# Kernel optimization log

Measured on AMD Instinct MI355X. Metric: run time of the kernel, lower is better.

Reference implementation:

```python
import jax, jax.numpy as jnp
import numpy as np

N, E = 100000, 1600000
IN_C, HID, OUT = 128, 64, 25
EPS = 1e-5


def gcn_conv(x, row, col, W, b):
    # PyG GCNConv: h = x@W; add self-loops; sym-norm D^-1/2 A D^-1/2; + bias
    h = x @ W                                   # [N, F]
    ones = jnp.ones(row.shape[0], h.dtype)
    deg = jax.ops.segment_sum(ones, col, num_segments=N) + 1.0  # +1 self-loop
    dinv = jax.lax.rsqrt(deg)                   # [N]
    norm = dinv[row] * dinv[col]                # [E]
    agg = jax.ops.segment_sum(h[row] * norm[:, None], col, num_segments=N)
    agg = agg + (dinv * dinv)[:, None] * h      # self-loop contribution
    return agg + b


def layer_norm(x, w, b):
    # PyG LayerNorm mode='node': normalize each node over feature dim
    mu = jnp.mean(x, axis=-1, keepdims=True)
    var = jnp.var(x, axis=-1, keepdims=True)
    return (x - mu) * jax.lax.rsqrt(var + EPS) * w + b


def setup_inputs() -> dict:
    key = jax.random.key(0)
    ks = jax.random.split(key, 16)
    x = jax.random.normal(ks[0], (N, IN_C), dtype=jnp.float32)
    edge_index = jax.random.randint(ks[1], (2, E), 0, N, dtype=jnp.int32)

    def glorot(k, shp):
        lim = float(np.sqrt(6.0 / (shp[0] + shp[1])))
        return jax.random.uniform(k, shp, jnp.float32, -lim, lim)

    return {
        "x": x,
        "edge_index": edge_index,
        "W1": glorot(ks[2], (IN_C, HID)), "b1": jnp.zeros((HID,), jnp.float32),
        "W2": glorot(ks[3], (HID, HID)), "b2": jnp.zeros((HID,), jnp.float32),
        "W3": glorot(ks[4], (HID, HID)), "b3": jnp.zeros((HID,), jnp.float32),
        "ln1_w": jnp.ones((HID,), jnp.float32), "ln1_b": jnp.zeros((HID,), jnp.float32),
        "ln2_w": jnp.ones((HID,), jnp.float32), "ln2_b": jnp.zeros((HID,), jnp.float32),
        "ln3_w": jnp.ones((HID,), jnp.float32), "ln3_b": jnp.zeros((HID,), jnp.float32),
        "Wl": glorot(ks[5], (HID, OUT)), "bl": jnp.zeros((OUT,), jnp.float32),
    }


def reference(x, edge_index, W1, b1, W2, b2, W3, b3,
              ln1_w, ln1_b, ln2_w, ln2_b, ln3_w, ln3_b, Wl, bl):
    row, col = edge_index[0], edge_index[1]
    h = jax.nn.relu(layer_norm(gcn_conv(x, row, col, W1, b1), ln1_w, ln1_b))
    h = jax.nn.relu(layer_norm(gcn_conv(h, row, col, W2, b2), ln2_w, ln2_b))
    h = jax.nn.relu(layer_norm(gcn_conv(h, row, col, W3, b3), ln3_w, ln3_b))
    pooled = jnp.mean(h, axis=0)                # [HID]
    return pooled @ Wl + bl                     # [OUT]
```

## Files before the change

kernel.cpp:

```cpp
#include <hip/hip_runtime.h>
#include <hip/hip_bf16.h>

typedef __hip_bfloat16 bf16;
typedef __attribute__((ext_vector_type(8))) short short8;
typedef __attribute__((ext_vector_type(4))) float f32x4;
typedef __attribute__((ext_vector_type(2))) float f32x2;

#define HID 64
#define CAP 4096
#define BSH 7
#define EPB 2048

__device__ __forceinline__ unsigned short f2bfbits(float x){
    union { float f; unsigned u; } c; c.f = x;
    unsigned r = c.u + 0x7fffu + ((c.u >> 16) & 1u);
    return (unsigned short)(r >> 16);
}
__device__ __forceinline__ unsigned char f2fp8(float x){
    unsigned v = __builtin_amdgcn_cvt_pk_fp8_f32(x, x, 0u, false);
    return (unsigned char)(v & 0xffu);
}
template<bool HI>
__device__ __forceinline__ f32x2 cvtpk(unsigned u){
    return __builtin_amdgcn_cvt_pk_f32_fp8(u, HI);
}


__global__ __launch_bounds__(1024) void bin_kernel(const int* __restrict__ row,
                                                   const int* __restrict__ col,
                                                   int E, int NB,
                                                   int* __restrict__ gCur,
                                                   int* __restrict__ binned,
                                                   unsigned char* __restrict__ H8a,
                                                   unsigned char* __restrict__ H8b,
                                                   int N){
    __shared__ int lCnt[1024];
    __shared__ int lOff[1024];
    __shared__ int lGB[1024];
    __shared__ int sPay[EPB];
    __shared__ unsigned short sB[EPB];
    __shared__ int wSum[16];
    int tid = threadIdx.x;
    int lane = tid & 63, wv = tid >> 6;
    if (blockIdx.x == 0 && tid < 32){
        unsigned* za = (unsigned*)(H8a + ((size_t)N << 6));
        unsigned* zb = (unsigned*)(H8b + ((size_t)N << 6));
        if (tid < 16) za[tid] = 0u; else zb[tid - 16] = 0u;
    }
    int e0 = blockIdx.x * EPB;
    int eN = E - e0; if (eN > EPB) eN = EPB;

    lCnt[tid] = 0;
    int cols[2], rows[2];
    #pragma unroll
    for (int k = 0; k < 2; ++k){
        int i = tid + k * 1024;
        bool ok = (i < eN);
        cols[k] = ok ? col[e0 + i] : -1;
        rows[k] = ok ? row[e0 + i] : 0;
    }
    __syncthreads();
    #pragma unroll
    for (int k = 0; k < 2; ++k)
        if (cols[k] >= 0) atomicAdd(&lCnt[cols[k] >> BSH], 1);
    __syncthreads();

    int c = lCnt[tid];
    int inc = c;
    #pragma unroll
    for (int m = 1; m < 64; m <<= 1){
        int t = __shfl_up(inc, m);
        if (lane >= m) inc += t;
    }
    if (lane == 63) wSum[wv] = inc;
    __syncthreads();
    if (wv == 0 && lane < 16){
        int orig = wSum[lane];
        int ws = orig;
        #pragma unroll
        for (int m = 1; m < 16; m <<= 1){
            int t = __shfl_up(ws, m);
            if (lane >= m) ws += t;
        }
        wSum[lane] = ws - orig;
    }
    __syncthreads();
    int excl = inc - c + wSum[wv];
    lOff[tid] = excl;
    if (c){
        int gb = atomicAdd(&gCur[tid], c);
        lGB[tid] = tid * CAP + gb - excl;
    }
    lCnt[tid] = 0;
    __syncthreads();

    #pragma unroll
    for (int k = 0; k < 2; ++k){
        if (cols[k] >= 0){
            int bk = cols[k] >> BSH;
            int rk = atomicAdd(&lCnt[bk], 1);
            int pos = lOff[bk] + rk;
            sPay[pos] = ((cols[k] & 127) << 17) | rows[k];
            sB[pos] = (unsigned short)bk;
        }
    }
    __syncthreads();

    #pragma unroll
    for (int k = 0; k < 2; ++k){
        int i = tid + k * 1024;
        if (i < eN){
            int bk = sB[i];
            int tgt = lGB[bk] + i;
            if (tgt - (bk << 12) < CAP)
                binned[tgt] = sPay[i];
        }
    }
}


template<int K, typename T>
__global__ __launch_bounds__(256) void matmul_kernel(const T* __restrict__ act,
                                                     const float* __restrict__ W,
                                                     const int* __restrict__ gCur,
                                                     const int* __restrict__ binned,
                                                     int* __restrict__ col_ptr,
                                                     int* __restrict__ cnt,
                                                     unsigned char* __restrict__ H8, int N){
    constexpr int KS = K / 32;
    constexpr int RB = 2 * K;
    __shared__ __align__(16) short As[128 * K];
    __shared__ __align__(16) short Wt[64 * K];
    __shared__ int fineCnt[128];
    __shared__ int scW[2];

    int tid = threadIdx.x;
    int b = blockIdx.x;
    int nodeBase = b * 128;
    int j0g = b * CAP;
    int cB = gCur[b];
    if (cB > CAP) cB = CAP;

    if (tid < 128) fineCnt[tid] = 0;

    for (int i = tid; i < K * 64; i += 256){
        int k = i >> 6, c = i & 63;
        unsigned short bb = f2bfbits(W[i]);
        int byte = c * RB + ((2 * k) ^ ((c & 7) << 4));
        *(short*)((char*)Wt + byte) = (short)bb;
    }
    constexpr int OPR = K / 8;
    for (int i = tid; i < 128 * OPR; i += 256){
        int node = i / OPR, oct = i % OPR;
        int n = nodeBase + node;
        short8 v = (short8)0;
        if (n < N){
            if constexpr (sizeof(T) == 4){
                const float4* xp = (const float4*)&act[(size_t)n * K + oct * 8];
                float4 a = xp[0], bb = xp[1];
                v[0] = (short)f2bfbits(a.x); v[1] = (short)f2bfbits(a.y);
                v[2] = (short)f2bfbits(a.z); v[3] = (short)f2bfbits(a.w);
                v[4] = (short)f2bfbits(bb.x); v[5] = (short)f2bfbits(bb.y);
                v[6] = (short)f2bfbits(bb.z); v[7] = (short)f2bfbits(bb.w);
            } else {
                v = *(const short8*)&act[(size_t)n * K + oct * 8];
            }
        }
        int byte = node * RB + ((oct * 16) ^ ((node & 7) << 4));
        *(short8*)((char*)As + byte) = v;
    }
    __syncthreads();

    for (int i = tid; i < cB; i += 256)
        atomicAdd(&fineCnt[binned[j0g + i] >> 17], 1);
    __syncthreads();
    int cf = 0, inc = 0;
    if (tid < 128){
        cf = fineCnt[tid];
        inc = cf;
        #pragma unroll
        for (int m = 1; m < 64; m <<= 1){
            int t = __shfl_up(inc, m);
            if ((tid & 63) >= m) inc += t;
        }
        if ((tid & 63) == 63) scW[tid >> 6] = inc;
    }
    __syncthreads();
    if (tid < 128){
        int off = (tid >= 64) ? scW[0] : 0;
        int node = nodeBase + tid;
        if (node < N){
            col_ptr[node] = j0g + off + inc - cf;
            cnt[node] = cf;
        }
    }
    __syncthreads();

    int wv = tid >> 6, l = tid & 63;
    int lr = l & 15, lg = l >> 4;

    short8 bfr[KS][4];
    #pragma unroll
    for (int ks = 0; ks < KS; ++ks)
        #pragma unroll
        for (int t = 0; t < 4; ++t){
            int c = t * 16 + lr;
            int byte = c * RB + ((ks * 64 + lg * 16) ^ ((c & 7) << 4));
            bfr[ks][t] = *(const short8*)((const char*)Wt + byte);
        }

    #pragma unroll
    for (int nt = 0; nt < 2; ++nt){
        int nb = wv * 32 + nt * 16;
        int node = nb + lr;
        short8 af[KS];
        #pragma unroll
        for (int ks = 0; ks < KS; ++ks){
            int byte = node * RB + ((ks * 64 + lg * 16) ^ ((node & 7) << 4));
            af[ks] = *(const short8*)((const char*)As + byte);
        }
        f32x4 acc[4] = {(f32x4)0.f, (f32x4)0.f, (f32x4)0.f, (f32x4)0.f};
        #pragma unroll
        for (int ks = 0; ks < KS; ++ks)
            #pragma unroll
            for (int t = 0; t < 4; ++t)
                acc[t] = __builtin_amdgcn_mfma_f32_16x16x32_bf16(af[ks], bfr[ks][t], acc[t], 0, 0, 0);
        #pragma unroll
        for (int r = 0; r < 4; ++r){
            int loc = nb + lg * 4 + r;
            int n = nodeBase + loc;
            if (n < N){
                float dv = rsqrtf((float)fineCnt[loc] + 1.0f);
                #pragma unroll
                for (int t = 0; t < 4; ++t)
                    H8[((size_t)(unsigned)n << 6) + t * 16 + lr] = f2fp8(acc[t][r] * dv);
            }
        }
    }
}


__global__ __launch_bounds__(512) void agg_sort_kernel(const unsigned char* __restrict__ H8in,
                                                       const int* __restrict__ cnt,
                                                       const int* __restrict__ gCur,
                                                       const int* __restrict__ binned,
                                                       const int* __restrict__ col_ptr,
                                                       int* __restrict__ csr_row,
                                                       const float* __restrict__ bias,
                                                       const float* __restrict__ lnw,
                                                       const float* __restrict__ lnb,
                                                       const float* __restrict__ Wn,
                                                       unsigned char* __restrict__ H8out,
                                                       int N){
    __shared__ int sCsr[CAP];
    __shared__ __align__(16) short ybuf[8192];
    __shared__ __align__(16) short Wt[4096];
    __shared__ int fineCur[128];
    __shared__ float sdv[128];
    int b = blockIdx.x, tid = threadIdx.x;
    int wid = tid >> 6, l = tid & 63;
    int g = l >> 2, s = l & 3;
    int nodeBase = b << BSH;
    int n = nodeBase + wid * 16 + g;
    bool valid = (n < N);
    int nc = valid ? n : N;

    int j0g = b * CAP;
    int cntB = gCur[b];
    if (cntB > CAP) cntB = CAP;

    for (int i = tid; i < 4096; i += 512){
        int k = i >> 6, c = i & 63;
        unsigned short bb = f2bfbits(Wn[i]);
        int byte = c * 128 + ((2 * k) ^ ((c & 7) << 4));
        *(short*)((char*)Wt + byte) = (short)bb;
    }
    if (tid < 128){
        int node = nodeBase + tid;
        fineCur[tid] = (node < N) ? (col_ptr[node] - j0g) : 0;
    }
    __syncthreads();

    for (int i = tid; i < cntB; i += 512){
        int w = binned[j0g + i];
        int pos = atomicAdd(&fineCur[w >> 17], 1);
        sCsr[pos] = w & 0x1FFFF;
    }
    __syncthreads();
    for (int i = tid; i < cntB; i += 512) csr_row[j0g + i] = sCsr[i];

    int deg = valid ? cnt[nc] : 0;
    int p = valid ? (col_ptr[nc] - j0g) : 0;
    unsigned soff = (unsigned)(s << 4);
    const char* Hb = (const char*)H8in;
    uint4 us = *(const uint4*)(Hb + ((((unsigned)nc) << 6) | soff));

    int mdeg = deg;
    mdeg = max(mdeg, __shfl_xor(mdeg, 4));
    mdeg = max(mdeg, __shfl_xor(mdeg, 8));
    mdeg = max(mdeg, __shfl_xor(mdeg, 16));
    mdeg = max(mdeg, __shfl_xor(mdeg, 32));

    f32x2 a0 = {0.f,0.f}, a1 = {0.f,0.f}, a2 = {0.f,0.f}, a3 = {0.f,0.f};
    f32x2 a4 = {0.f,0.f}, a5 = {0.f,0.f}, a6 = {0.f,0.f}, a7 = {0.f,0.f};
#define ACC4(u) { a0 += cvtpk<false>((u).x); a1 += cvtpk<true>((u).x); \
                  a2 += cvtpk<false>((u).y); a3 += cvtpk<true>((u).y); \
                  a4 += cvtpk<false>((u).z); a5 += cvtpk<true>((u).z); \
                  a6 += cvtpk<false>((u).w); a7 += cvtpk<true>((u).w); }
    for (int i = 0; i < mdeg; i += 4){
        int r0 = (i     < deg) ? sCsr[p + i    ] : N;
        int r1 = (i + 1 < deg) ? sCsr[p + i + 1] : N;
        int r2 = (i + 2 < deg) ? sCsr[p + i + 2] : N;
        int r3 = (i + 3 < deg) ? sCsr[p + i + 3] : N;
        uint4 u0 = *(const uint4*)(Hb + ((((unsigned)r0) << 6) | soff));
        uint4 u1 = *(const uint4*)(Hb + ((((unsigned)r1) << 6) | soff));
        uint4 u2 = *(const uint4*)(Hb + ((((unsigned)r2) << 6) | soff));
        uint4 u3 = *(const uint4*)(Hb + ((((unsigned)r3) << 6) | soff));
        ACC4(u0) ACC4(u1) ACC4(u2) ACC4(u3)
    }
#undef ACC4
    a0 += cvtpk<false>(us.x); a1 += cvtpk<true>(us.x);
    a2 += cvtpk<false>(us.y); a3 += cvtpk<true>(us.y);
    a4 += cvtpk<false>(us.z); a5 += cvtpk<true>(us.z);
    a6 += cvtpk<false>(us.w); a7 += cvtpk<true>(us.w);

    float dv = rsqrtf((float)deg + 1.0f);
    float acc16[16] = { a0.x, a0.y, a1.x, a1.y, a2.x, a2.y, a3.x, a3.y,
                        a4.x, a4.y, a5.x, a5.y, a6.x, a6.y, a7.x, a7.y };
    float v[16], y[16];
    float4 bq[4], wq[4], cq[4];
    #pragma unroll
    for (int q = 0; q < 4; ++q){
        bq[q] = ((const float4*)bias)[(s << 2) + q];
        wq[q] = ((const float4*)lnw)[(s << 2) + q];
        cq[q] = ((const float4*)lnb)[(s << 2) + q];
    }
    #pragma unroll
    for (int j = 0; j < 16; ++j)
        v[j] = fmaf(dv, acc16[j], ((const float*)&bq[j >> 2])[j & 3]);
    float sum = 0.f;
    #pragma unroll
    for (int j = 0; j < 16; ++j) sum += v[j];
    sum += __shfl_xor(sum, 1); sum += __shfl_xor(sum, 2);
    float mu = sum * (1.0f / 64.0f);
    float var = 0.f;
    #pragma unroll
    for (int j = 0; j < 16; ++j){ float d = v[j] - mu; var = fmaf(d, d, var); }
    var += __shfl_xor(var, 1); var += __shfl_xor(var, 2);
    float rstd = rsqrtf(var * (1.0f / 64.0f) + 1e-5f);
    #pragma unroll
    for (int j = 0; j < 16; ++j){
        float d = (v[j] - mu) * rstd;
        y[j] = fmaxf(fmaf(d, ((const float*)&wq[j >> 2])[j & 3],
                             ((const float*)&cq[j >> 2])[j & 3]), 0.0f);
    }

    if (s == 0) sdv[(wid << 4) + g] = dv;
    char* yb = (char*)ybuf;
    int base = (wid << 11) + (g << 7);
    int sw = (g & 7) << 4;
    short8 ya, yz;
    #pragma unroll
    for (int j = 0; j < 8; ++j){ ya[j] = (short)f2bfbits(y[j]); yz[j] = (short)f2bfbits(y[8 + j]); }
    *(short8*)(yb + base + (((s << 5)     ) ^ sw)) = ya;
    *(short8*)(yb + base + (((s << 5) + 16) ^ sw)) = yz;

    int lr = l & 15, lg = l >> 4;
    short8 bfr[2][4];
    #pragma unroll
    for (int ks = 0; ks < 2; ++ks)
        #pragma unroll
        for (int t = 0; t < 4; ++t){
            int c = t * 16 + lr;
            int byte = c * 128 + ((((ks << 2) + lg) << 4) ^ ((c & 7) << 4));
            bfr[ks][t] = *(const short8*)((const char*)Wt + byte);
        }
    short8 af[2];
    #pragma unroll
    for (int ks = 0; ks < 2; ++ks){
        int byte = (wid << 11) + lr * 128 + ((((ks << 2) + lg) << 4) ^ ((lr & 7) << 4));
        af[ks] = *(const short8*)(yb + byte);
    }
    f32x4 acc[4] = {(f32x4)0.f, (f32x4)0.f, (f32x4)0.f, (f32x4)0.f};
    #pragma unroll
    for (int ks = 0; ks < 2; ++ks)
        #pragma unroll
        for (int t = 0; t < 4; ++t)
            acc[t] = __builtin_amdgcn_mfma_f32_16x16x32_bf16(af[ks], bfr[ks][t], acc[t], 0, 0, 0);
    #pragma unroll
    for (int r = 0; r < 4; ++r){
        int nn = nodeBase + (wid << 4) + (lg << 2) + r;
        if (nn < N){
            float dv2 = sdv[(wid << 4) + (lg << 2) + r];
            #pragma unroll
            for (int t = 0; t < 4; ++t)
                H8out[((size_t)(unsigned)nn << 6) + t * 16 + lr] = f2fp8(acc[t][r] * dv2);
        }
    }
}


template<bool POOL>
__global__ __launch_bounds__(256) void agg_kernel(const unsigned char* __restrict__ H8in,
                                                  const int* __restrict__ cnt,
                                                  const int* __restrict__ col_ptr,
                                                  const int* __restrict__ csr_row,
                                                  const float* __restrict__ bias,
                                                  const float* __restrict__ lnw,
                                                  const float* __restrict__ lnb,
                                                  const float* __restrict__ Wn,
                                                  unsigned char* __restrict__ H8out,
                                                  float* __restrict__ pooledRep, int N){
    __shared__ int sIdx[CAP];
    __shared__ __align__(16) short ybuf[POOL ? 8 : 4096];
    __shared__ __align__(16) short Wt[POOL ? 8 : 4096];
    __shared__ float sp[POOL ? 256 : 4];
    __shared__ float sdv[64];
    int tid = threadIdx.x;
    int wid = tid >> 6, l = tid & 63;
    int g = l >> 2, s = l & 3;
    int nodeBase = blockIdx.x * 64;
    int n = nodeBase + wid * 16 + g;
    bool valid = (n < N);
    int nc = valid ? n : N;

    int lastN = nodeBase + 63; if (lastN > N - 1) lastN = N - 1;
    int jlo = col_ptr[nodeBase];
    int jhi = col_ptr[lastN] + cnt[lastN];
    int cntR = jhi - jlo;

    int deg = valid ? cnt[n] : 0;
    int p = valid ? (col_ptr[n] - jlo) : 0;

    for (int i = tid; i < cntR; i += 256) sIdx[i] = csr_row[jlo + i];
    if (!POOL){
        for (int i = tid; i < 4096; i += 256){
            int k = i >> 6, c = i & 63;
            unsigned short bb = f2bfbits(Wn[i]);
            int byte = c * 128 + ((2 * k) ^ ((c & 7) << 4));
            *(short*)((char*)Wt + byte) = (short)bb;
        }
    }
    __syncthreads();

    unsigned soff = (unsigned)(s << 4);
    const char* Hb = (const char*)H8in;
    uint4 us = *(const uint4*)(Hb + ((((unsigned)nc) << 6) | soff));

    int mdeg = deg;
    mdeg = max(mdeg, __shfl_xor(mdeg, 4));
    mdeg = max(mdeg, __shfl_xor(mdeg, 8));
    mdeg = max(mdeg, __shfl_xor(mdeg, 16));
    mdeg = max(mdeg, __shfl_xor(mdeg, 32));

    f32x2 a0 = {0.f,0.f}, a1 = {0.f,0.f}, a2 = {0.f,0.f}, a3 = {0.f,0.f};
    f32x2 a4 = {0.f,0.f}, a5 = {0.f,0.f}, a6 = {0.f,0.f}, a7 = {0.f,0.f};
#define ACC4(u) { a0 += cvtpk<false>((u).x); a1 += cvtpk<true>((u).x); \
                  a2 += cvtpk<false>((u).y); a3 += cvtpk<true>((u).y); \
                  a4 += cvtpk<false>((u).z); a5 += cvtpk<true>((u).z); \
                  a6 += cvtpk<false>((u).w); a7 += cvtpk<true>((u).w); }
    for (int i = 0; i < mdeg; i += 4){
        int r0 = (i     < deg) ? sIdx[p + i    ] : N;
        int r1 = (i + 1 < deg) ? sIdx[p + i + 1] : N;
        int r2 = (i + 2 < deg) ? sIdx[p + i + 2] : N;
        int r3 = (i + 3 < deg) ? sIdx[p + i + 3] : N;
        uint4 u0 = *(const uint4*)(Hb + ((((unsigned)r0) << 6) | soff));
        uint4 u1 = *(const uint4*)(Hb + ((((unsigned)r1) << 6) | soff));
        uint4 u2 = *(const uint4*)(Hb + ((((unsigned)r2) << 6) | soff));
        uint4 u3 = *(const uint4*)(Hb + ((((unsigned)r3) << 6) | soff));
        ACC4(u0) ACC4(u1) ACC4(u2) ACC4(u3)
    }
#undef ACC4
    a0 += cvtpk<false>(us.x); a1 += cvtpk<true>(us.x);
    a2 += cvtpk<false>(us.y); a3 += cvtpk<true>(us.y);
    a4 += cvtpk<false>(us.z); a5 += cvtpk<true>(us.z);
    a6 += cvtpk<false>(us.w); a7 += cvtpk<true>(us.w);

    float dv = rsqrtf((float)deg + 1.0f);
    float acc16[16] = { a0.x, a0.y, a1.x, a1.y, a2.x, a2.y, a3.x, a3.y,
                        a4.x, a4.y, a5.x, a5.y, a6.x, a6.y, a7.x, a7.y };
    float v[16], y[16];
    float4 bq[4], wq[4], cq[4];
    #pragma unroll
    for (int q = 0; q < 4; ++q){
        bq[q] = ((const float4*)bias)[(s << 2) + q];
        wq[q] = ((const float4*)lnw)[(s << 2) + q];
        cq[q] = ((const float4*)lnb)[(s << 2) + q];
    }
    #pragma unroll
    for (int j = 0; j < 16; ++j)
        v[j] = fmaf(dv, acc16[j], ((const float*)&bq[j >> 2])[j & 3]);
    float sum = 0.f;
    #pragma unroll
    for (int j = 0; j < 16; ++j) sum += v[j];
    sum += __shfl_xor(sum, 1); sum += __shfl_xor(sum, 2);
    float mu = sum * (1.0f / 64.0f);
    float var = 0.f;
    #pragma unroll
    for (int j = 0; j < 16; ++j){ float d = v[j] - mu; var = fmaf(d, d, var); }
    var += __shfl_xor(var, 1); var += __shfl_xor(var, 2);
    float rstd = rsqrtf(var * (1.0f / 64.0f) + 1e-5f);
    #pragma unroll
    for (int j = 0; j < 16; ++j){
        float d = (v[j] - mu) * rstd;
        y[j] = fmaxf(fmaf(d, ((const float*)&wq[j >> 2])[j & 3],
                             ((const float*)&cq[j >> 2])[j & 3]), 0.0f);
    }

    if (POOL){
        #pragma unroll
        for (int j = 0; j < 16; ++j){
            float z = valid ? y[j] : 0.f;
            z += __shfl_xor(z, 4); z += __shfl_xor(z, 8);
            z += __shfl_xor(z, 16); z += __shfl_xor(z, 32);
            y[j] = z;
        }
        if (l < 4){
            #pragma unroll
            for (int q = 0; q < 4; ++q)
                ((float4*)sp)[wid * 16 + (s << 2) + q] =
                    make_float4(y[4*q], y[4*q+1], y[4*q+2], y[4*q+3]);
        }
        __syncthreads();
        if (tid < 64){
            float t = sp[tid] + sp[64 + tid] + sp[128 + tid] + sp[192 + tid];
            atomicAdd(&pooledRep[(blockIdx.x & 63) * 64 + tid], t);
        }
    } else {
        if (s == 0) sdv[(wid << 4) + g] = dv;
        char* yb = (char*)ybuf;
        int base = (wid << 11) + (g << 7);
        int sw = (g & 7) << 4;
        short8 ya, yz;
        #pragma unroll
        for (int j = 0; j < 8; ++j){ ya[j] = (short)f2bfbits(y[j]); yz[j] = (short)f2bfbits(y[8 + j]); }
        *(short8*)(yb + base + (((s << 5)     ) ^ sw)) = ya;
        *(short8*)(yb + base + (((s << 5) + 16) ^ sw)) = yz;

        int lr = l & 15, lg = l >> 4;
        short8 bfr[2][4];
        #pragma unroll
        for (int ks = 0; ks < 2; ++ks)
            #pragma unroll
            for (int t = 0; t < 4; ++t){
                int c = t * 16 + lr;
                int byte = c * 128 + ((((ks << 2) + lg) << 4) ^ ((c & 7) << 4));
                bfr[ks][t] = *(const short8*)((const char*)Wt + byte);
            }
        short8 af[2];
        #pragma unroll
        for (int ks = 0; ks < 2; ++ks){
            int byte = (wid << 11) + lr * 128 + ((((ks << 2) + lg) << 4) ^ ((lr & 7) << 4));
            af[ks] = *(const short8*)(yb + byte);
        }
        f32x4 acc[4] = {(f32x4)0.f, (f32x4)0.f, (f32x4)0.f, (f32x4)0.f};
        #pragma unroll
        for (int ks = 0; ks < 2; ++ks)
            #pragma unroll
            for (int t = 0; t < 4; ++t)
                acc[t] = __builtin_amdgcn_mfma_f32_16x16x32_bf16(af[ks], bfr[ks][t], acc[t], 0, 0, 0);
        #pragma unroll
        for (int r = 0; r < 4; ++r){
            int nn = nodeBase + (wid << 4) + (lg << 2) + r;
            if (nn < N){
                float dv2 = sdv[(wid << 4) + (lg << 2) + r];
                #pragma unroll
                for (int t = 0; t < 4; ++t)
                    H8out[((size_t)(unsigned)nn << 6) + t * 16 + lr] = f2fp8(acc[t][r] * dv2);
            }
        }
    }
}


__global__ __launch_bounds__(64) void final_kernel(const float* __restrict__ pooledRep,
                                                   const float* __restrict__ Wl,
                                                   const float* __restrict__ bl,
                                                   float* __restrict__ outp, float invN){
    __shared__ float pooled[64];
    int t = threadIdx.x;
    float s = 0.f;
    #pragma unroll 8
    for (int r = 0; r < 64; ++r) s += pooledRep[r * 64 + t];
    pooled[t] = s;
    __syncthreads();
    if (t < 25){
        float acc = bl[t];
        #pragma unroll 8
        for (int f = 0; f < HID; ++f)
            acc = fmaf(pooled[f] * invN, Wl[f * 25 + t], acc);
        outp[t] = acc;
    }
}


static inline size_t alignup(size_t x){ return (x + 255) & ~(size_t)255; }

extern "C" void kernel_launch(void* const* d_in, const int* in_sizes, int n_in,
                              void* d_out, int out_size, void* d_ws, size_t ws_size,
                              hipStream_t stream) {
    const float* x   = (const float*)d_in[0];
    const int*   ei  = (const int*)d_in[1];
    const float* W1  = (const float*)d_in[2];
    const float* b1  = (const float*)d_in[3];
    const float* W2  = (const float*)d_in[4];
    const float* b2  = (const float*)d_in[5];
    const float* W3  = (const float*)d_in[6];
    const float* b3  = (const float*)d_in[7];
    const float* ln1w = (const float*)d_in[8];
    const float* ln1b = (const float*)d_in[9];
    const float* ln2w = (const float*)d_in[10];
    const float* ln2b = (const float*)d_in[11];
    const float* ln3w = (const float*)d_in[12];
    const float* ln3b = (const float*)d_in[13];
    const float* Wl  = (const float*)d_in[14];
    const float* bl  = (const float*)d_in[15];

    const int N = in_sizes[0] / 128;
    const int E = in_sizes[1] / 2;
    const int NB = (N + 127) >> BSH;
    const int* row = ei;
    const int* col = ei + E;

    char* p = (char*)d_ws;
    int*   gCur      = (int*)p;   p += alignup((size_t)NB * 4);
    float* pooledRep = (float*)p; p += alignup(64 * 64 * 4);
    size_t zeroBytes = (size_t)((char*)p - (char*)gCur);
    int*   binned    = (int*)p;   p += alignup((size_t)NB * CAP * 4);
    int*   csr_row   = (int*)p;   p += alignup((size_t)NB * CAP * 4);
    int*   col_ptr   = (int*)p;   p += alignup((size_t)N * 4);
    int*   cnt       = (int*)p;   p += alignup((size_t)N * 4);
    unsigned char* H8a = (unsigned char*)p; p += alignup(((size_t)N + 1) * HID);
    unsigned char* H8b = (unsigned char*)p; p += alignup(((size_t)N + 1) * HID);

    hipMemsetAsync(gCur, 0, zeroBytes, stream);

    int gB = (E + EPB - 1) / EPB;
    int gM = (N + 127) / 128;
    int gA = (N + 63) / 64;

    bin_kernel<<<gB, 1024, 0, stream>>>(row, col, E, NB, gCur, binned, H8a, H8b, N);

    matmul_kernel<128, float><<<gM, 256, 0, stream>>>(x, W1, gCur, binned,
                                                      col_ptr, cnt, H8a, N);
    agg_sort_kernel<<<NB, 512, 0, stream>>>(H8a, cnt, gCur, binned, col_ptr, csr_row,
                                            b1, ln1w, ln1b, W2, H8b, N);
    agg_kernel<false><<<gA, 256, 0, stream>>>(H8b, cnt, col_ptr, csr_row,
                                              b2, ln2w, ln2b, W3, H8a, pooledRep, N);
    agg_kernel<true><<<gA, 256, 0, stream>>>(H8a, cnt, col_ptr, csr_row,
                                             b3, ln3w, ln3b, nullptr, nullptr, pooledRep, N);

    final_kernel<<<1, 64, 0, stream>>>(pooledRep, Wl, bl, (float*)d_out, 1.0f / (float)N);
}
```

Baseline: 241.3 us.

## Unify aggregation kernels, rebuild CSR per layer in LDS, fuse final linear

All three GCN aggregation layers now use one templated 512-thread kernel that re-sorts the binned edges into shared memory each time, rather than writing a global csr_row array and reloading it in later layers. The final pooling plus linear projection is folded into the last layer with a last-block-done atomic counter, which removes the separate final kernel launch. The gather loop is unrolled to eight neighbors per iteration to keep more loads in flight. In exchange, each layer repeats the LDS sort work and uses larger blocks with more shared memory, which may lower occupancy.

```diff
diff --git a/kernel.cpp b/kernel.cpp
--- a/kernel.cpp
+++ b/kernel.cpp
@@ -240,23 +240,30 @@
 }
 
 
-__global__ __launch_bounds__(512) void agg_sort_kernel(const unsigned char* __restrict__ H8in,
-                                                       const int* __restrict__ cnt,
-                                                       const int* __restrict__ gCur,
-                                                       const int* __restrict__ binned,
-                                                       const int* __restrict__ col_ptr,
-                                                       int* __restrict__ csr_row,
-                                                       const float* __restrict__ bias,
-                                                       const float* __restrict__ lnw,
-                                                       const float* __restrict__ lnb,
-                                                       const float* __restrict__ Wn,
-                                                       unsigned char* __restrict__ H8out,
-                                                       int N){
+template<int EPI>
+__global__ __launch_bounds__(512) void agg_kernel(const unsigned char* __restrict__ H8in,
+                                                  const int* __restrict__ cnt,
+                                                  const int* __restrict__ gCur,
+                                                  const int* __restrict__ binned,
+                                                  const int* __restrict__ col_ptr,
+                                                  const float* __restrict__ bias,
+                                                  const float* __restrict__ lnw,
+                                                  const float* __restrict__ lnb,
+                                                  const float* __restrict__ Wn,
+                                                  unsigned char* __restrict__ H8out,
+                                                  float* __restrict__ pooledRep,
+                                                  const float* __restrict__ Wl,
+                                                  const float* __restrict__ bl,
+                                                  float* __restrict__ outp,
+                                                  int* __restrict__ done,
+                                                  float invN, int N){
     __shared__ int sCsr[CAP];
-    __shared__ __align__(16) short ybuf[8192];
-    __shared__ __align__(16) short Wt[4096];
+    __shared__ __align__(16) short ybuf[EPI ? 8 : 8192];
+    __shared__ __align__(16) short Wt[EPI ? 8 : 4096];
+    __shared__ float sp[EPI ? 512 : 4];
     __shared__ int fineCur[128];
     __shared__ float sdv[128];
+    __shared__ int isLast;
     int b = blockIdx.x, tid = threadIdx.x;
     int wid = tid >> 6, l = tid & 63;
     int g = l >> 2, s = l & 3;
@@ -269,11 +276,13 @@
     int cntB = gCur[b];
     if (cntB > CAP) cntB = CAP;
 
-    for (int i = tid; i < 4096; i += 512){
-        int k = i >> 6, c = i & 63;
-        unsigned short bb = f2bfbits(Wn[i]);
-        int byte = c * 128 + ((2 * k) ^ ((c & 7) << 4));
-        *(short*)((char*)Wt + byte) = (short)bb;
+    if (EPI == 0){
+        for (int i = tid; i < 4096; i += 512){
+            int k = i >> 6, c = i & 63;
+            unsigned short bb = f2bfbits(Wn[i]);
+            int byte = c * 128 + ((2 * k) ^ ((c & 7) << 4));
+            *(short*)((char*)Wt + byte) = (short)bb;
+        }
     }
     if (tid < 128){
         int node = nodeBase + tid;
@@ -287,7 +296,6 @@
         sCsr[pos] = w & 0x1FFFF;
     }
     __syncthreads();
-    for (int i = tid; i < cntB; i += 512) csr_row[j0g + i] = sCsr[i];
 
     int deg = valid ? cnt[nc] : 0;
     int p = valid ? (col_ptr[nc] - j0g) : 0;
@@ -307,16 +315,15 @@
                   a2 += cvtpk<false>((u).y); a3 += cvtpk<true>((u).y); \
                   a4 += cvtpk<false>((u).z); a5 += cvtpk<true>((u).z); \
                   a6 += cvtpk<false>((u).w); a7 += cvtpk<true>((u).w); }
-    for (int i = 0; i < mdeg; i += 4){
-        int r0 = (i     < deg) ? sCsr[p + i    ] : N;
-        int r1 = (i + 1 < deg) ? sCsr[p + i + 1] : N;
-        int r2 = (i + 2 < deg) ? sCsr[p + i + 2] : N;
-        int r3 = (i + 3 < deg) ? sCsr[p + i + 3] : N;
-        uint4 u0 = *(const uint4*)(Hb + ((((unsigned)r0) << 6) | soff));
-        uint4 u1 = *(const uint4*)(Hb + ((((unsigned)r1) << 6) | soff));
-        uint4 u2 = *(const uint4*)(Hb + ((((unsigned)r2) << 6) | soff));
-        uint4 u3 = *(const uint4*)(Hb + ((((unsigned)r3) << 6) | soff));
-        ACC4(u0) ACC4(u1) ACC4(u2) ACC4(u3)
+    for (int i = 0; i < mdeg; i += 8){
+        uint4 u[8];
+        #pragma unroll
+        for (int t = 0; t < 8; ++t){
+            int r = (i + t < deg) ? sCsr[p + i + t] : N;
+            u[t] = *(const uint4*)(Hb + ((((unsigned)r) << 6) | soff));
+        }
+        #pragma unroll
+        for (int t = 0; t < 8; ++t) ACC4(u[t])
     }
 #undef ACC4
     a0 += cvtpk<false>(us.x); a1 += cvtpk<true>(us.x);
@@ -355,159 +362,7 @@
                              ((const float*)&cq[j >> 2])[j & 3]), 0.0f);
     }
 
-    if (s == 0) sdv[(wid << 4) + g] = dv;
-    char* yb = (char*)ybuf;
-    int base = (wid << 11) + (g << 7);
-    int sw = (g & 7) << 4;
-    short8 ya, yz;
-    #pragma unroll
-    for (int j = 0; j < 8; ++j){ ya[j] = (short)f2bfbits(y[j]); yz[j] = (short)f2bfbits(y[8 + j]); }
-    *(short8*)(yb + base + (((s << 5)     ) ^ sw)) = ya;
-    *(short8*)(yb + base + (((s << 5) + 16) ^ sw)) = yz;
-
-    int lr = l & 15, lg = l >> 4;
-    short8 bfr[2][4];
-    #pragma unroll
-    for (int ks = 0; ks < 2; ++ks)
-        #pragma unroll
-        for (int t = 0; t < 4; ++t){
-            int c = t * 16 + lr;
-            int byte = c * 128 + ((((ks << 2) + lg) << 4) ^ ((c & 7) << 4));
-            bfr[ks][t] = *(const short8*)((const char*)Wt + byte);
-        }
-    short8 af[2];
-    #pragma unroll
-    for (int ks = 0; ks < 2; ++ks){
-        int byte = (wid << 11) + lr * 128 + ((((ks << 2) + lg) << 4) ^ ((lr & 7) << 4));
-        af[ks] = *(const short8*)(yb + byte);
-    }
-    f32x4 acc[4] = {(f32x4)0.f, (f32x4)0.f, (f32x4)0.f, (f32x4)0.f};
-    #pragma unroll
-    for (int ks = 0; ks < 2; ++ks)
-        #pragma unroll
-        for (int t = 0; t < 4; ++t)
-            acc[t] = __builtin_amdgcn_mfma_f32_16x16x32_bf16(af[ks], bfr[ks][t], acc[t], 0, 0, 0);
-    #pragma unroll
-    for (int r = 0; r < 4; ++r){
-        int nn = nodeBase + (wid << 4) + (lg << 2) + r;
-        if (nn < N){
-            float dv2 = sdv[(wid << 4) + (lg << 2) + r];
-            #pragma unroll
-            for (int t = 0; t < 4; ++t)
-                H8out[((size_t)(unsigned)nn << 6) + t * 16 + lr] = f2fp8(acc[t][r] * dv2);
-        }
-    }
-}
-
-
-template<bool POOL>
-__global__ __launch_bounds__(256) void agg_kernel(const unsigned char* __restrict__ H8in,
-                                                  const int* __restrict__ cnt,
-                                                  const int* __restrict__ col_ptr,
-                                                  const int* __restrict__ csr_row,
-                                                  const float* __restrict__ bias,
-                                                  const float* __restrict__ lnw,
-                                                  const float* __restrict__ lnb,
-                                                  const float* __restrict__ Wn,
-                                                  unsigned char* __restrict__ H8out,
-                                                  float* __restrict__ pooledRep, int N){
-    __shared__ int sIdx[CAP];
-    __shared__ __align__(16) short ybuf[POOL ? 8 : 4096];
-    __shared__ __align__(16) short Wt[POOL ? 8 : 4096];
-    __shared__ float sp[POOL ? 256 : 4];
-    __shared__ float sdv[64];
-    int tid = threadIdx.x;
-    int wid = tid >> 6, l = tid & 63;
-    int g = l >> 2, s = l & 3;
-    int nodeBase = blockIdx.x * 64;
-    int n = nodeBase + wid * 16 + g;
-    bool valid = (n < N);
-    int nc = valid ? n : N;
-
-    int lastN = nodeBase + 63; if (lastN > N - 1) lastN = N - 1;
-    int jlo = col_ptr[nodeBase];
-    int jhi = col_ptr[lastN] + cnt[lastN];
-    int cntR = jhi - jlo;
-
-    int deg = valid ? cnt[n] : 0;
-    int p = valid ? (col_ptr[n] - jlo) : 0;
-
-    for (int i = tid; i < cntR; i += 256) sIdx[i] = csr_row[jlo + i];
-    if (!POOL){
-        for (int i = tid; i < 4096; i += 256){
-            int k = i >> 6, c = i & 63;
-            unsigned short bb = f2bfbits(Wn[i]);
-            int byte = c * 128 + ((2 * k) ^ ((c & 7) << 4));
-            *(short*)((char*)Wt + byte) = (short)bb;
-        }
-    }
-    __syncthreads();
-
-    unsigned soff = (unsigned)(s << 4);
-    const char* Hb = (const char*)H8in;
-    uint4 us = *(const uint4*)(Hb + ((((unsigned)nc) << 6) | soff));
-
-    int mdeg = deg;
-    mdeg = max(mdeg, __shfl_xor(mdeg, 4));
-    mdeg = max(mdeg, __shfl_xor(mdeg, 8));
-    mdeg = max(mdeg, __shfl_xor(mdeg, 16));
-    mdeg = max(mdeg, __shfl_xor(mdeg, 32));
-
-    f32x2 a0 = {0.f,0.f}, a1 = {0.f,0.f}, a2 = {0.f,0.f}, a3 = {0.f,0.f};
-    f32x2 a4 = {0.f,0.f}, a5 = {0.f,0.f}, a6 = {0.f,0.f}, a7 = {0.f,0.f};
-#define ACC4(u) { a0 += cvtpk<false>((u).x); a1 += cvtpk<true>((u).x); \
-                  a2 += cvtpk<false>((u).y); a3 += cvtpk<true>((u).y); \
-                  a4 += cvtpk<false>((u).z); a5 += cvtpk<true>((u).z); \
-                  a6 += cvtpk<false>((u).w); a7 += cvtpk<true>((u).w); }
-    for (int i = 0; i < mdeg; i += 4){
-        int r0 = (i     < deg) ? sIdx[p + i    ] : N;
-        int r1 = (i + 1 < deg) ? sIdx[p + i + 1] : N;
-        int r2 = (i + 2 < deg) ? sIdx[p + i + 2] : N;
-        int r3 = (i + 3 < deg) ? sIdx[p + i + 3] : N;
-        uint4 u0 = *(const uint4*)(Hb + ((((unsigned)r0) << 6) | soff));
-        uint4 u1 = *(const uint4*)(Hb + ((((unsigned)r1) << 6) | soff));
-        uint4 u2 = *(const uint4*)(Hb + ((((unsigned)r2) << 6) | soff));
-        uint4 u3 = *(const uint4*)(Hb + ((((unsigned)r3) << 6) | soff));
-        ACC4(u0) ACC4(u1) ACC4(u2) ACC4(u3)
-    }
-#undef ACC4
-    a0 += cvtpk<false>(us.x); a1 += cvtpk<true>(us.x);
-    a2 += cvtpk<false>(us.y); a3 += cvtpk<true>(us.y);
-    a4 += cvtpk<false>(us.z); a5 += cvtpk<true>(us.z);
-    a6 += cvtpk<false>(us.w); a7 += cvtpk<true>(us.w);
-
-    float dv = rsqrtf((float)deg + 1.0f);
-    float acc16[16] = { a0.x, a0.y, a1.x, a1.y, a2.x, a2.y, a3.x, a3.y,
-                        a4.x, a4.y, a5.x, a5.y, a6.x, a6.y, a7.x, a7.y };
-    float v[16], y[16];
-    float4 bq[4], wq[4], cq[4];
-    #pragma unroll
-    for (int q = 0; q < 4; ++q){
-        bq[q] = ((const float4*)bias)[(s << 2) + q];
-        wq[q] = ((const float4*)lnw)[(s << 2) + q];
-        cq[q] = ((const float4*)lnb)[(s << 2) + q];
-    }
-    #pragma unroll
-    for (int j = 0; j < 16; ++j)
-        v[j] = fmaf(dv, acc16[j], ((const float*)&bq[j >> 2])[j & 3]);
-    float sum = 0.f;
-    #pragma unroll
-    for (int j = 0; j < 16; ++j) sum += v[j];
-    sum += __shfl_xor(sum, 1); sum += __shfl_xor(sum, 2);
-    float mu = sum * (1.0f / 64.0f);
-    float var = 0.f;
-    #pragma unroll
-    for (int j = 0; j < 16; ++j){ float d = v[j] - mu; var = fmaf(d, d, var); }
-    var += __shfl_xor(var, 1); var += __shfl_xor(var, 2);
-    float rstd = rsqrtf(var * (1.0f / 64.0f) + 1e-5f);
-    #pragma unroll
-    for (int j = 0; j < 16; ++j){
-        float d = (v[j] - mu) * rstd;
-        y[j] = fmaxf(fmaf(d, ((const float*)&wq[j >> 2])[j & 3],
-                             ((const float*)&cq[j >> 2])[j & 3]), 0.0f);
-    }
-
-    if (POOL){
+    if (EPI == 1){
         #pragma unroll
         for (int j = 0; j < 16; ++j){
             float z = valid ? y[j] : 0.f;
@@ -523,8 +378,31 @@
         }
         __syncthreads();
         if (tid < 64){
-            float t = sp[tid] + sp[64 + tid] + sp[128 + tid] + sp[192 + tid];
-            atomicAdd(&pooledRep[(blockIdx.x & 63) * 64 + tid], t);
+            float t = 0.f;
+            #pragma unroll
+            for (int w = 0; w < 8; ++w) t += sp[w * 64 + tid];
+            atomicAdd(&pooledRep[(b & 63) * 64 + tid], t);
+        }
+        __threadfence();
+        __syncthreads();
+        if (tid == 0) isLast = (atomicAdd(done, 1) == (int)gridDim.x - 1);
+        __syncthreads();
+        if (isLast){
+            __threadfence();
+            if (tid < 64){
+                float ssum = 0.f;
+                #pragma unroll 8
+                for (int r = 0; r < 64; ++r) ssum += pooledRep[r * 64 + tid];
+                sp[tid] = ssum;
+            }
+            __syncthreads();
+            if (tid < 25){
+                float acc2 = bl[tid];
+                #pragma unroll 8
+                for (int f = 0; f < HID; ++f)
+                    acc2 = fmaf(sp[f] * invN, Wl[f * 25 + tid], acc2);
+                outp[tid] = acc2;
+            }
         }
     } else {
         if (s == 0) sdv[(wid << 4) + g] = dv;
@@ -569,27 +447,6 @@
                     H8out[((size_t)(unsigned)nn << 6) + t * 16 + lr] = f2fp8(acc[t][r] * dv2);
             }
         }
-    }
-}
-
-
-__global__ __launch_bounds__(64) void final_kernel(const float* __restrict__ pooledRep,
-                                                   const float* __restrict__ Wl,
-                                                   const float* __restrict__ bl,
-                                                   float* __restrict__ outp, float invN){
-    __shared__ float pooled[64];
-    int t = threadIdx.x;
-    float s = 0.f;
-    #pragma unroll 8
-    for (int r = 0; r < 64; ++r) s += pooledRep[r * 64 + t];
-    pooled[t] = s;
-    __syncthreads();
-    if (t < 25){
-        float acc = bl[t];
-        #pragma unroll 8
-        for (int f = 0; f < HID; ++f)
-            acc = fmaf(pooled[f] * invN, Wl[f * 25 + t], acc);
-        outp[t] = acc;
     }
 }
 
@@ -625,9 +482,9 @@
     char* p = (char*)d_ws;
     int*   gCur      = (int*)p;   p += alignup((size_t)NB * 4);
     float* pooledRep = (float*)p; p += alignup(64 * 64 * 4);
+    int*   done      = (int*)p;   p += alignup(4);
     size_t zeroBytes = (size_t)((char*)p - (char*)gCur);
     int*   binned    = (int*)p;   p += alignup((size_t)NB * CAP * 4);
-    int*   csr_row   = (int*)p;   p += alignup((size_t)NB * CAP * 4);
     int*   col_ptr   = (int*)p;   p += alignup((size_t)N * 4);
     int*   cnt       = (int*)p;   p += alignup((size_t)N * 4);
     unsigned char* H8a = (unsigned char*)p; p += alignup(((size_t)N + 1) * HID);
@@ -637,18 +494,19 @@
 
     int gB = (E + EPB - 1) / EPB;
     int gM = (N + 127) / 128;
-    int gA = (N + 63) / 64;
+    float invN = 1.0f / (float)N;
 
     bin_kernel<<<gB, 1024, 0, stream>>>(row, col, E, NB, gCur, binned, H8a, H8b, N);
 
     matmul_kernel<128, float><<<gM, 256, 0, stream>>>(x, W1, gCur, binned,
                                                       col_ptr, cnt, H8a, N);
-    agg_sort_kernel<<<NB, 512, 0, stream>>>(H8a, cnt, gCur, binned, col_ptr, csr_row,
-                                            b1, ln1w, ln1b, W2, H8b, N);
-    agg_kernel<false><<<gA, 256, 0, stream>>>(H8b, cnt, col_ptr, csr_row,
-                                              b2, ln2w, ln2b, W3, H8a, pooledRep, N);
-    agg_kernel<true><<<gA, 256, 0, stream>>>(H8a, cnt, col_ptr, csr_row,
-                                             b3, ln3w, ln3b, nullptr, nullptr, pooledRep, N);
-
-    final_kernel<<<1, 64, 0, stream>>>(pooledRep, Wl, bl, (float*)d_out, 1.0f / (float)N);
-}
+    agg_kernel<0><<<NB, 512, 0, stream>>>(H8a, cnt, gCur, binned, col_ptr,
+                                          b1, ln1w, ln1b, W2, H8b, pooledRep,
+                                          nullptr, nullptr, nullptr, done, invN, N);
+    agg_kernel<0><<<NB, 512, 0, stream>>>(H8b, cnt, gCur, binned, col_ptr,
+                                          b2, ln2w, ln2b, W3, H8a, pooledRep,
+                                          nullptr, nullptr, nullptr, done, invN, N);
+    agg_kernel<1><<<NB, 512, 0, stream>>>(H8a, cnt, gCur, binned, col_ptr,
+                                          b3, ln3w, ln3b, nullptr, nullptr, pooledRep,
+                                          Wl, bl, (float*)d_out, done, invN, N);
+}
```

Result: slower. 354.6 us (+46.9%).
